# Optimization experiments

Hardware: AMD Instinct MI355X
Metric: run time of the kernel (lower is better)

Reference implementation:

```python
import jax, jax.numpy as jnp
import numpy as np

N_NODES = 100000
N_EDGES = 1600000
N_FEAT = 64
EXP_FEAT = 50
CUTOFF = 5.0
LOG2 = float(np.log(2.0))


def ssp(x):
    # ShiftedSoftplus: softplus(x) - log(2)
    return jax.nn.softplus(x) - LOG2


def setup_inputs() -> dict:
    key = jax.random.key(0)
    ks = jax.random.split(key, 16)
    s = 1.0 / np.sqrt(N_FEAT)
    se = 1.0 / np.sqrt(EXP_FEAT)
    return {
        "neighbour_index": jax.random.randint(ks[0], (2, N_EDGES), 0, N_NODES, dtype=jnp.int64)
        if jax.config.read("jax_enable_x64") else jax.random.randint(ks[0], (2, N_EDGES), 0, N_NODES, dtype=jnp.int32),
        "neighbour_distances": jax.random.uniform(ks[1], (N_EDGES,), jnp.float32) * CUTOFF,
        "node_features": jax.random.normal(ks[2], (N_NODES, N_FEAT), jnp.float32),
        # initial linear transform
        "lin_w": jax.random.uniform(ks[3], (N_FEAT, N_FEAT), jnp.float32, -s, s),
        "lin_b": jax.random.uniform(ks[4], (N_FEAT,), jnp.float32, -s, s),
        # filter MLP: [EXP_FEAT -> N_FEAT -> N_FEAT], ssp between layers
        "f_w1": jax.random.uniform(ks[5], (N_FEAT, EXP_FEAT), jnp.float32, -se, se),
        "f_b1": jax.random.uniform(ks[6], (N_FEAT,), jnp.float32, -se, se),
        "f_w2": jax.random.uniform(ks[7], (N_FEAT, N_FEAT), jnp.float32, -s, s),
        "f_b2": jax.random.uniform(ks[8], (N_FEAT,), jnp.float32, -s, s),
        # output MLP: [N_FEAT -> N_FEAT -> N_FEAT]
        "m_w1": jax.random.uniform(ks[9], (N_FEAT, N_FEAT), jnp.float32, -s, s),
        "m_b1": jax.random.uniform(ks[10], (N_FEAT,), jnp.float32, -s, s),
        "m_w2": jax.random.uniform(ks[11], (N_FEAT, N_FEAT), jnp.float32, -s, s),
        "m_b2": jax.random.uniform(ks[12], (N_FEAT,), jnp.float32, -s, s),
    }


def reference(neighbour_index, neighbour_distances, node_features,
              lin_w, lin_b, f_w1, f_b1, f_w2, f_b2,
              m_w1, m_b1, m_w2, m_b2):
    n_nodes = node_features.shape[0]
    src = neighbour_index[0]  # j (messages gathered from)
    dst = neighbour_index[1]  # i (messages aggregated into)

    # h_i <- W x_i
    h = node_features @ lin_w.T + lin_b  # [N, F]

    # Gaussian smearing of distances: [E, K]
    centers = jnp.linspace(0.0, CUTOFF, EXP_FEAT, dtype=node_features.dtype)
    delta = centers[1] - centers[0]
    coeff = -0.5 / (delta * delta)
    rbf = jnp.exp(coeff * (neighbour_distances[:, None] - centers[None, :]) ** 2)

    # filter MLP F(r_ij): [E, F]
    filt = ssp(rbf @ f_w1.T + f_b1) @ f_w2.T + f_b2

    # message m_ij = h_j * F(r_ij); scatter-add into targets
    msg = h[src] * filt  # [E, F]
    agg = jax.ops.segment_sum(msg, dst, num_segments=n_nodes)  # [N, F]

    # output MLP
    return ssp(agg @ m_w1.T + m_b1) @ m_w2.T + m_b2
```

## Files before the change

### kernel.cpp

```cpp
#include <hip/hip_runtime.h>
#include <hip/hip_fp16.h>

#define NF 64
#define KEXP 50
#define TBL 16384
#define CUTF 5.0f
#define LOG2C 0.6931471805599453f
#define GRP 32
#define GSH 5
#define NSC 256
#define GMAX 4096
#define SCAP 768
#define RPT (SCAP / 256)

typedef unsigned long long ull;
typedef _Float16 f16x8 __attribute__((ext_vector_type(8)));
typedef float f32x4 __attribute__((ext_vector_type(4)));

__device__ __forceinline__ float sspf(float x) {
    return fmaxf(x, 0.0f) + __logf(1.0f + __expf(-fabsf(x))) - LOG2C;
}

__device__ __forceinline__ f16x8 load_wfrag(const float* __restrict__ w, int f, int k0) {
    const float4 q0 = *(const float4*)(w + (size_t)f * NF + k0);
    const float4 q1 = *(const float4*)(w + (size_t)f * NF + k0 + 4);
    f16x8 r;
    r[0] = (_Float16)q0.x; r[1] = (_Float16)q0.y; r[2] = (_Float16)q0.z; r[3] = (_Float16)q0.w;
    r[4] = (_Float16)q1.x; r[5] = (_Float16)q1.y; r[6] = (_Float16)q1.z; r[7] = (_Float16)q1.w;
    return r;
}

__device__ __forceinline__ f16x8 load_afrag_f32(const float* __restrict__ p) {
    const float4 q0 = *(const float4*)(p);
    const float4 q1 = *(const float4*)(p + 4);
    f16x8 r;
    r[0] = (_Float16)q0.x; r[1] = (_Float16)q0.y; r[2] = (_Float16)q0.z; r[3] = (_Float16)q0.w;
    r[4] = (_Float16)q1.x; r[5] = (_Float16)q1.y; r[6] = (_Float16)q1.z; r[7] = (_Float16)q1.w;
    return r;
}

__global__ void __launch_bounds__(256) build_tabnn_k(
    const float* __restrict__ f_w1, const float* __restrict__ f_b1,
    const float* __restrict__ f_w2, const float* __restrict__ f_b2,
    __half* __restrict__ tabnn) {
    const int tid = threadIdx.x;
    const int lane = tid & 63;
    const int wid = tid >> 6;
    float w1r[KEXP], w2r[NF];
    for (int k = 0; k < KEXP; ++k) w1r[k] = f_w1[lane * KEXP + k];
    for (int k = 0; k < NF; ++k)  w2r[k] = f_w2[lane * NF + k];
    const float b1 = f_b1[lane], b2 = f_b2[lane];
    const float delta = CUTF / (float)(KEXP - 1);
    const float coeff = -0.5f / (delta * delta);
    const float dstep = CUTF / (float)(TBL - 1);
    for (int tt = 0; tt < 16; ++tt) {
        const int t = blockIdx.x * 64 + wid * 16 + tt;
        const float d = (float)t * dstep;
        float rbfv = 0.f;
        if (lane < KEXP) {
            const float dd = d - (float)lane * delta;
            rbfv = __expf(coeff * dd * dd);
        }
        float t1 = b1;
        for (int k = 0; k < KEXP; ++k) t1 = fmaf(__shfl(rbfv, k), w1r[k], t1);
        const float sv = sspf(t1);
        float t2 = b2;
        for (int k = 0; k < NF; ++k) t2 = fmaf(__shfl(sv, k), w2r[k], t2);
        tabnn[(size_t)t * NF + lane] = __float2half(t2);
    }
}

__global__ void __launch_bounds__(256) front_k(
    const int* __restrict__ nbr_dst, int n_edges, int ngroups, int chk,
    unsigned* __restrict__ cnt,
    const float* __restrict__ x, const float* __restrict__ w,
    const float* __restrict__ b, __half* __restrict__ h16, int n_nodes)
{
    __shared__ __align__(16) char smem[GMAX * 4];
    const int blk = blockIdx.x;
    const int tid = threadIdx.x;
    const int lane = tid & 63;
    const int wid = tid >> 6;

    if (blk < NSC) {
        unsigned* cnt_s = (unsigned*)smem;
        const int c = blk;
        const int e0 = c * chk;
        const int e1 = min(e0 + chk, n_edges);
        const int m = max(e1 - e0, 0);
        for (int g = tid; g < ngroups; g += 256) cnt_s[g] = 0u;
        __syncthreads();
        for (int i = tid; i < m; i += 256)
            atomicAdd(&cnt_s[(unsigned)nbr_dst[e0 + i] >> GSH], 1u);
        __syncthreads();
        const size_t ob = (size_t)c * ngroups;
        for (int g = tid; g < ngroups; g += 256) cnt[ob + g] = cnt_s[g];
    } else {
        _Float16 (*stile)[16][72] = (_Float16(*)[16][72])smem;
        const int col = lane & 15;
        const int quad = lane >> 4;
        f16x8 bw[4][2];
        float bv[4];
        #pragma unroll
        for (int t = 0; t < 4; ++t) {
            #pragma unroll
            for (int kb = 0; kb < 2; ++kb)
                bw[t][kb] = load_wfrag(w, 16 * t + col, kb * 32 + quad * 8);
            bv[t] = b[16 * t + col];
        }
        const int pb = blk - NSC;
        const int pgrid = gridDim.x - NSC;
        const int ntiles = (n_nodes + 15) >> 4;
        for (int tile = pb * 4 + wid; tile < ntiles; tile += pgrid * 4) {
            const int n0 = tile << 4;
            const int nr = min(n0 + col, n_nodes - 1);
            f16x8 a[2];
            #pragma unroll
            for (int kb = 0; kb < 2; ++kb)
                a[kb] = load_afrag_f32(x + (size_t)nr * NF + kb * 32 + quad * 8);
            f32x4 acc[4];
            #pragma unroll
            for (int t = 0; t < 4; ++t) acc[t] = (f32x4){bv[t], bv[t], bv[t], bv[t]};
            #pragma unroll
            for (int t = 0; t < 4; ++t)
                #pragma unroll
                for (int kb = 0; kb < 2; ++kb)
                    acc[t] = __builtin_amdgcn_mfma_f32_16x16x32_f16(a[kb], bw[t][kb], acc[t], 0, 0, 0);
            #pragma unroll
            for (int t = 0; t < 4; ++t)
                #pragma unroll
                for (int r = 0; r < 4; ++r)
                    stile[wid][quad * 4 + r][16 * t + col] = (_Float16)acc[t][r];
            __threadfence_block();
            #pragma unroll
            for (int it = 0; it < 2; ++it) {
                const int chunk = it * 64 + lane;
                const int row = chunk >> 3;
                const int off = (chunk & 7) * 8;
                const int n = n0 + row;
                if (n < n_nodes)
                    *(uint4*)(h16 + (size_t)n * NF + off) = *(const uint4*)&stile[wid][row][off];
            }
            __threadfence_block();
        }
    }
}

__global__ void __launch_bounds__(64) colscan_k(const unsigned* __restrict__ cnt,
                                                unsigned* __restrict__ colpre,
                                                unsigned* __restrict__ tot, int ngroups) {
    const int g = blockIdx.x;
    const int lane = threadIdx.x;
    unsigned v[4];
    unsigned s = 0u;
    #pragma unroll
    for (int j = 0; j < 4; ++j) {
        v[j] = cnt[(size_t)(4 * lane + j) * ngroups + g];
        s += v[j];
    }
    unsigned run = s;
    #pragma unroll
    for (int d = 1; d < 64; d <<= 1) {
        const unsigned t = __shfl_up(run, d, 64);
        if (lane >= d) run += t;
    }
    unsigned pre = run - s;
    #pragma unroll
    for (int j = 0; j < 4; ++j) {
        colpre[(size_t)(4 * lane + j) * ngroups + g] = pre;
        pre += v[j];
    }
    if (lane == 63) tot[g] = run;
}

__global__ void __launch_bounds__(64) base_k(const unsigned* __restrict__ tot,
                                             unsigned* __restrict__ gbase, int ngroups) {
    const int lane = threadIdx.x;
    unsigned carry = 0u;
    for (int base = 0; base < ngroups; base += 64) {
        const int g = base + lane;
        const unsigned v = (g < ngroups) ? tot[g] : 0u;
        unsigned run = v;
        #pragma unroll
        for (int d = 1; d < 64; d <<= 1) {
            const unsigned t = __shfl_up(run, d, 64);
            if (lane >= d) run += t;
        }
        if (g < ngroups) gbase[g] = carry + run - v;
        carry += (unsigned)__shfl((int)run, 63, 64);
    }
    if (lane == 0) gbase[ngroups] = carry;
}

__global__ void __launch_bounds__(1024) scatter2_k(const int* __restrict__ nbr,
                                                   const float* __restrict__ dist,
                                                   int n_edges, int ngroups, int chk,
                                                   const unsigned* __restrict__ colpre,
                                                   const unsigned* __restrict__ gbase,
                                                   ull* __restrict__ payload) {
    __shared__ unsigned cur_s[GMAX];
    const int tid = threadIdx.x;
    const int c = blockIdx.x;
    const int e0 = c * chk;
    const int e1 = min(e0 + chk, n_edges);
    const int m = max(e1 - e0, 0);
    const size_t ob = (size_t)c * ngroups;
    for (int g = tid; g < ngroups; g += 1024) cur_s[g] = gbase[g] + colpre[ob + g];
    __syncthreads();
    const float scale = (float)(TBL - 1) / CUTF;
    for (int i = tid; i < m; i += 1024) {
        const int e = e0 + i;
        const unsigned dst = (unsigned)nbr[n_edges + e];
        const unsigned src = (unsigned)nbr[e];
        const float xx = dist[e] * scale + 0.5f;
        int i0 = (int)xx;
        i0 = max(0, min(i0, TBL - 1));
        const ull rec = (ull)((unsigned)i0 << 7) |
                        ((ull)((src << 7) | (dst & (GRP - 1u))) << 32);
        const unsigned pos = atomicAdd(&cur_s[dst >> GSH], 1u);
        payload[pos] = rec;
    }
}

__global__ void __launch_bounds__(256) agg_k(
    const ull* __restrict__ payload, const unsigned* __restrict__ gbase,
    const __half* __restrict__ h16, const __half* __restrict__ tabnn,
    float* __restrict__ agg, int n_nodes)
{
    __shared__ ull sorted_s[SCAP];
    __shared__ unsigned cnt_s[GRP];
    __shared__ unsigned base_s[GRP];
    __shared__ unsigned cur_s[GRP];
    const int tid = threadIdx.x;
    const int lane = tid & 63;
    const int wid = tid >> 6;
    const int g = blockIdx.x;
    const unsigned beg = gbase[g];
    const unsigned end = gbase[g + 1];
    const unsigned tot = min(end - beg, (unsigned)SCAP);

    if (tid < GRP) cnt_s[tid] = 0u;
    __syncthreads();
    ull rec[RPT];
    #pragma unroll
    for (int k = 0; k < RPT; ++k) {
        const unsigned i = (unsigned)(k * 256) + tid;
        rec[k] = 0ull;
        if (i < tot) {
            rec[k] = payload[beg + i];
            atomicAdd(&cnt_s[(unsigned)(rec[k] >> 32) & (GRP - 1u)], 1u);
        }
    }
    __syncthreads();
    if (tid < GRP) {
        const unsigned c = cnt_s[tid];
        unsigned run = c;
        #pragma unroll
        for (int d = 1; d < GRP; d <<= 1) {
            const unsigned t = __shfl_up(run, d, 64);
            if (tid >= d) run += t;
        }
        base_s[tid] = run - c;
        cur_s[tid]  = run - c;
    }
    __syncthreads();
    #pragma unroll
    for (int k = 0; k < RPT; ++k) {
        const unsigned i = (unsigned)(k * 256) + tid;
        if (i < tot) {
            const unsigned pos = atomicAdd(&cur_s[(unsigned)(rec[k] >> 32) & (GRP - 1u)], 1u);
            sorted_s[pos] = rec[k];
        }
    }
    __syncthreads();
    const char* tabB = (const char*)tabnn + (lane << 1);
    const char* hB   = (const char*)h16 + (lane << 1);
    auto ev = [&](ull r) -> float {
        const unsigned lo = (unsigned)r;
        const unsigned hi = (unsigned)(r >> 32);
        const float tv = __half2float(*(const __half*)(tabB + lo));
        const float hv = __half2float(*(const __half*)(hB + (hi & 0xFFFFFF80u)));
        return tv * hv;
    };
    const int n0 = g * GRP;
    for (int rr = 0; rr < GRP / 4; ++rr) {
        const int r = wid * (GRP / 4) + rr;
        unsigned i = base_s[r];
        const unsigned e = cur_s[r];
        float acc0 = 0.f, acc1 = 0.f;
        for (; i + 16u <= e; i += 16u) {
            ull rv[16];
            #pragma unroll
            for (int j = 0; j < 16; ++j) rv[j] = sorted_s[i + j];
            float p[16];
            #pragma unroll
            for (int j = 0; j < 16; ++j) p[j] = ev(rv[j]);
            acc0 += ((p[0] + p[1]) + (p[2] + p[3])) + ((p[4] + p[5]) + (p[6] + p[7]));
            acc1 += ((p[8] + p[9]) + (p[10] + p[11])) + ((p[12] + p[13]) + (p[14] + p[15]));
        }
        for (; i + 4u <= e; i += 4u) {
            const ull r0 = sorted_s[i];
            const ull r1 = sorted_s[i + 1];
            const ull r2 = sorted_s[i + 2];
            const ull r3 = sorted_s[i + 3];
            acc0 += ev(r0) + ev(r1);
            acc1 += ev(r2) + ev(r3);
        }
        for (; i < e; ++i) acc0 += ev(sorted_s[i]);
        const int n = n0 + r;
        if (n < n_nodes) agg[(size_t)n * NF + lane] = acc0 + acc1;
    }
}

__global__ void __launch_bounds__(64) oflow2_k(const ull* __restrict__ payload,
                                               const unsigned* __restrict__ gbase,
                                               const __half* __restrict__ h16,
                                               const __half* __restrict__ tabnn,
                                               float* __restrict__ agg) {
    const int g = blockIdx.x;
    const unsigned beg = gbase[g];
    const unsigned end = gbase[g + 1];
    if (end - beg <= (unsigned)SCAP) return;
    const int lane = threadIdx.x;
    const char* tabB = (const char*)tabnn + (lane << 1);
    const char* hB   = (const char*)h16 + (lane << 1);
    for (unsigned i = beg + SCAP; i < end; ++i) {
        const ull rec = payload[i];
        const unsigned lo = (unsigned)rec;
        const unsigned hi = (unsigned)(rec >> 32);
        const float tv = __half2float(*(const __half*)(tabB + lo));
        const float hv = __half2float(*(const __half*)(hB + (hi & 0xFFFFFF80u)));
        const unsigned row = (unsigned)g * GRP + (hi & (GRP - 1u));
        atomicAdd(agg + (size_t)row * NF + lane, tv * hv);
    }
}

__global__ void edge_k(const int* __restrict__ nbr, const float* __restrict__ dist,
                       const __half* __restrict__ h16, const __half* __restrict__ tabnn,
                       float* __restrict__ agg, int n_edges) {
    const int tid = threadIdx.x;
    const int lane = tid & 63;
    const int nwaves = (gridDim.x * blockDim.x) >> 6;
    const int gw = (blockIdx.x * blockDim.x + tid) >> 6;
    const float scale = (float)(TBL - 1) / CUTF;
    const int nbatch = n_edges >> 6;
    for (int bb = gw; bb < nbatch; bb += nwaves) {
        const int e0 = bb << 6;
        int src = nbr[e0 + lane];
        int dst = nbr[n_edges + e0 + lane];
        float d = dist[e0 + lane];
        float xx = d * scale + 0.5f;
        int i0 = (int)xx;
        i0 = max(0, min(i0, TBL - 1));
        #pragma unroll 4
        for (int j = 0; j < 64; ++j) {
            const int sj = __shfl(src, j);
            const int dj = __shfl(dst, j);
            const int ij = __shfl(i0, j);
            const float tv = __half2float(tabnn[(size_t)ij * NF + lane]);
            const float hv = __half2float(h16[(size_t)sj * NF + lane]);
            atomicAdd(agg + (size_t)dj * NF + lane, tv * hv);
        }
    }
    if (gw == 0) {
        for (int e = nbatch << 6; e < n_edges; ++e) {
            const int sj = nbr[e];
            const int dj = nbr[n_edges + e];
            const float d = dist[e];
            float xx = d * scale + 0.5f;
            int ij = (int)xx;
            ij = max(0, min(ij, TBL - 1));
            const float tv = __half2float(tabnn[(size_t)ij * NF + lane]);
            const float hv = __half2float(h16[(size_t)sj * NF + lane]);
            atomicAdd(agg + (size_t)dj * NF + lane, tv * hv);
        }
    }
}

__global__ void __launch_bounds__(256) out_mlp_k(const float* __restrict__ agg,
                                                 const float* __restrict__ w1,
                                                 const float* __restrict__ b1,
                                                 const float* __restrict__ w2,
                                                 const float* __restrict__ b2,
                                                 float* __restrict__ out, int n_nodes) {
    __shared__ _Float16 stile[4][16][72];
    const int tid = threadIdx.x;
    const int lane = tid & 63;
    const int wid = tid >> 6;
    const int col = lane & 15;
    const int quad = lane >> 4;

    f16x8 bw1[4][2], bw2[4][2];
    float b1v[4], b2v[4];
    #pragma unroll
    for (int t = 0; t < 4; ++t) {
        #pragma unroll
        for (int kb = 0; kb < 2; ++kb) {
            bw1[t][kb] = load_wfrag(w1, 16 * t + col, kb * 32 + quad * 8);
            bw2[t][kb] = load_wfrag(w2, 16 * t + col, kb * 32 + quad * 8);
        }
        b1v[t] = b1[16 * t + col];
        b2v[t] = b2[16 * t + col];
    }

    const int ntiles = (n_nodes + 15) >> 4;
    for (int tile = blockIdx.x * 4 + wid; tile < ntiles; tile += gridDim.x * 4) {
        const int n0 = tile << 4;
        const int nr = min(n0 + col, n_nodes - 1);
        f16x8 a[2];
        #pragma unroll
        for (int kb = 0; kb < 2; ++kb)
            a[kb] = load_afrag_f32(agg + (size_t)nr * NF + kb * 32 + quad * 8);
        f32x4 acc[4];
        #pragma unroll
        for (int t = 0; t < 4; ++t) acc[t] = (f32x4){b1v[t], b1v[t], b1v[t], b1v[t]};
        #pragma unroll
        for (int t = 0; t < 4; ++t)
            #pragma unroll
            for (int kb = 0; kb < 2; ++kb)
                acc[t] = __builtin_amdgcn_mfma_f32_16x16x32_f16(a[kb], bw1[t][kb], acc[t], 0, 0, 0);
        #pragma unroll
        for (int t = 0; t < 4; ++t)
            #pragma unroll
            for (int r = 0; r < 4; ++r)
                stile[wid][quad * 4 + r][16 * t + col] = (_Float16)sspf(acc[t][r]);
        __threadfence_block();
        f16x8 a2[2];
        #pragma unroll
        for (int kb = 0; kb < 2; ++kb)
            a2[kb] = *(const f16x8*)&stile[wid][col][kb * 32 + quad * 8];
        f32x4 acc2[4];
        #pragma unroll
        for (int t = 0; t < 4; ++t) acc2[t] = (f32x4){b2v[t], b2v[t], b2v[t], b2v[t]};
        #pragma unroll
        for (int t = 0; t < 4; ++t)
            #pragma unroll
            for (int kb = 0; kb < 2; ++kb)
                acc2[t] = __builtin_amdgcn_mfma_f32_16x16x32_f16(a2[kb], bw2[t][kb], acc2[t], 0, 0, 0);
        #pragma unroll
        for (int t = 0; t < 4; ++t)
            #pragma unroll
            for (int r = 0; r < 4; ++r) {
                const int n = n0 + quad * 4 + r;
                if (n < n_nodes) out[(size_t)n * NF + 16 * t + col] = acc2[t][r];
            }
        __threadfence_block();
    }
}

extern "C" void kernel_launch(void* const* d_in, const int* in_sizes, int n_in,
                              void* d_out, int out_size, void* d_ws, size_t ws_size,
                              hipStream_t stream) {
    const int*   nbr   = (const int*)d_in[0];
    const float* dist  = (const float*)d_in[1];
    const float* x     = (const float*)d_in[2];
    const float* lin_w = (const float*)d_in[3];
    const float* lin_b = (const float*)d_in[4];
    const float* f_w1  = (const float*)d_in[5];
    const float* f_b1  = (const float*)d_in[6];
    const float* f_w2  = (const float*)d_in[7];
    const float* f_b2  = (const float*)d_in[8];
    const float* m_w1  = (const float*)d_in[9];
    const float* m_b1  = (const float*)d_in[10];
    const float* m_w2  = (const float*)d_in[11];
    const float* m_b2  = (const float*)d_in[12];

    const int n_edges = in_sizes[1];
    const int n_nodes = in_sizes[2] / NF;
    const int ngroups = (n_nodes + GRP - 1) / GRP;
    const int chk     = (n_edges + NSC - 1) / NSC;
    const int ntiles  = (n_nodes + 15) / 16;
    const int mlp_blk = (ntiles + 3) / 4;

    float* out = (float*)d_out;
    float* agg = out;

    char* ws = (char*)d_ws;
    size_t off = 0;
    auto alloc = [&](size_t bytes) { char* p = ws + off; off = (off + bytes + 255) & ~(size_t)255; return p; };
    __half*   h16     = (__half*)alloc((size_t)n_nodes * NF * sizeof(__half));
    __half*   tabnn   = (__half*)alloc((size_t)TBL * NF * sizeof(__half));
    unsigned* cnt     = (unsigned*)alloc((size_t)NSC * ngroups * sizeof(unsigned));
    unsigned* colpre  = (unsigned*)alloc((size_t)NSC * ngroups * sizeof(unsigned));
    unsigned* tot     = (unsigned*)alloc((size_t)ngroups * sizeof(unsigned));
    unsigned* gbase   = (unsigned*)alloc((size_t)(ngroups + 1) * sizeof(unsigned));
    ull*      payload = (ull*)alloc((size_t)NSC * chk * sizeof(ull));
    const bool sort_path = (off <= ws_size) && (ngroups <= GMAX) && (n_nodes <= (1 << 17));

    build_tabnn_k<<<TBL / 64, 256, 0, stream>>>(f_w1, f_b1, f_w2, f_b2, tabnn);
    front_k<<<NSC + mlp_blk, 256, 0, stream>>>(
        nbr + n_edges, n_edges, ngroups, chk, cnt,
        x, lin_w, lin_b, h16, n_nodes);

    if (sort_path) {
        colscan_k<<<ngroups, 64, 0, stream>>>(cnt, colpre, tot, ngroups);
        base_k<<<1, 64, 0, stream>>>(tot, gbase, ngroups);
        scatter2_k<<<NSC, 1024, 0, stream>>>(nbr, dist, n_edges, ngroups, chk,
                                             colpre, gbase, payload);
        agg_k<<<ngroups, 256, 0, stream>>>(payload, gbase, h16, tabnn, agg, n_nodes);
        oflow2_k<<<ngroups, 64, 0, stream>>>(payload, gbase, h16, tabnn, agg);
    } else {
        hipMemsetAsync(agg, 0, (size_t)n_nodes * NF * sizeof(float), stream);
        edge_k<<<2048, 256, 0, stream>>>(nbr, dist, h16, tabnn, agg, n_edges);
    }
    out_mlp_k<<<mlp_blk, 256, 0, stream>>>(agg, m_w1, m_b1, m_w2, m_b2, out, n_nodes);
}
```

Before: 193.2 us.

## Fuse output MLP and overflow handling into the aggregation kernel

The aggregation kernel now keeps per-group aggregates in shared memory, folds overflow edges in with shared-memory atomics, and then runs the two-layer output MLP with MFMA on two waves before writing the final output. This removes the separate overflow kernel, the out_mlp kernel launch, and the global write and reread of the aggregate buffer. In exchange, shared memory use per block rises, and only two of four waves do the MLP work, which may lengthen the block tail.

```diff
diff --git a/kernel.cpp b/kernel.cpp
--- a/kernel.cpp
+++ b/kernel.cpp
@@ -30,7 +30,7 @@
     return r;
 }
 
-__device__ __forceinline__ f16x8 load_afrag_f32(const float* __restrict__ p) {
+__device__ __forceinline__ f16x8 load_afrag_f32(const float* p) {
     const float4 q0 = *(const float4*)(p);
     const float4 q1 = *(const float4*)(p + 4);
     f16x8 r;
@@ -222,12 +222,16 @@
     }
 }
 
-__global__ void __launch_bounds__(256) agg_k(
+__global__ void __launch_bounds__(256) agg_mlp_k(
     const ull* __restrict__ payload, const unsigned* __restrict__ gbase,
     const __half* __restrict__ h16, const __half* __restrict__ tabnn,
-    float* __restrict__ agg, int n_nodes)
+    const float* __restrict__ w1, const float* __restrict__ b1,
+    const float* __restrict__ w2, const float* __restrict__ b2,
+    float* __restrict__ out, int n_nodes)
 {
     __shared__ ull sorted_s[SCAP];
+    __shared__ float aggf[GRP][NF + 4];
+    __shared__ _Float16 hs[2][16][72];
     __shared__ unsigned cnt_s[GRP];
     __shared__ unsigned base_s[GRP];
     __shared__ unsigned cur_s[GRP];
@@ -282,7 +286,6 @@
         const float hv = __half2float(*(const __half*)(hB + (hi & 0xFFFFFF80u)));
         return tv * hv;
     };
-    const int n0 = g * GRP;
     for (int rr = 0; rr < GRP / 4; ++rr) {
         const int r = wid * (GRP / 4) + rr;
         unsigned i = base_s[r];
@@ -307,31 +310,70 @@
             acc1 += ev(r2) + ev(r3);
         }
         for (; i < e; ++i) acc0 += ev(sorted_s[i]);
-        const int n = n0 + r;
-        if (n < n_nodes) agg[(size_t)n * NF + lane] = acc0 + acc1;
-    }
-}
-
-__global__ void __launch_bounds__(64) oflow2_k(const ull* __restrict__ payload,
-                                               const unsigned* __restrict__ gbase,
-                                               const __half* __restrict__ h16,
-                                               const __half* __restrict__ tabnn,
-                                               float* __restrict__ agg) {
-    const int g = blockIdx.x;
-    const unsigned beg = gbase[g];
-    const unsigned end = gbase[g + 1];
-    if (end - beg <= (unsigned)SCAP) return;
-    const int lane = threadIdx.x;
-    const char* tabB = (const char*)tabnn + (lane << 1);
-    const char* hB   = (const char*)h16 + (lane << 1);
-    for (unsigned i = beg + SCAP; i < end; ++i) {
-        const ull rec = payload[i];
-        const unsigned lo = (unsigned)rec;
-        const unsigned hi = (unsigned)(rec >> 32);
-        const float tv = __half2float(*(const __half*)(tabB + lo));
-        const float hv = __half2float(*(const __half*)(hB + (hi & 0xFFFFFF80u)));
-        const unsigned row = (unsigned)g * GRP + (hi & (GRP - 1u));
-        atomicAdd(agg + (size_t)row * NF + lane, tv * hv);
+        aggf[r][lane] = acc0 + acc1;
+    }
+    __syncthreads();
+    if (end - beg > (unsigned)SCAP) {
+        for (unsigned i = (unsigned)SCAP + (unsigned)wid; i < end - beg; i += 4u) {
+            const ull r = payload[beg + i];
+            const unsigned row = (unsigned)(r >> 32) & (GRP - 1u);
+            atomicAdd(&aggf[row][lane], ev(r));
+        }
+        __syncthreads();
+    }
+    if (wid < 2) {
+        const int col = lane & 15;
+        const int quad = lane >> 4;
+        f16x8 bw1r[4][2], bw2r[4][2];
+        float b1v[4], b2v[4];
+        #pragma unroll
+        for (int t = 0; t < 4; ++t) {
+            #pragma unroll
+            for (int kb = 0; kb < 2; ++kb) {
+                bw1r[t][kb] = load_wfrag(w1, 16 * t + col, kb * 32 + quad * 8);
+                bw2r[t][kb] = load_wfrag(w2, 16 * t + col, kb * 32 + quad * 8);
+            }
+            b1v[t] = b1[16 * t + col];
+            b2v[t] = b2[16 * t + col];
+        }
+        f16x8 a[2];
+        #pragma unroll
+        for (int kb = 0; kb < 2; ++kb)
+            a[kb] = load_afrag_f32(&aggf[wid * 16 + col][kb * 32 + quad * 8]);
+        f32x4 acc[4];
+        #pragma unroll
+        for (int t = 0; t < 4; ++t) acc[t] = (f32x4){b1v[t], b1v[t], b1v[t], b1v[t]};
+        #pragma unroll
+        for (int t = 0; t < 4; ++t)
+            #pragma unroll
+            for (int kb = 0; kb < 2; ++kb)
+                acc[t] = __builtin_amdgcn_mfma_f32_16x16x32_f16(a[kb], bw1r[t][kb], acc[t], 0, 0, 0);
+        #pragma unroll
+        for (int t = 0; t < 4; ++t)
+            #pragma unroll
+            for (int r = 0; r < 4; ++r)
+                hs[wid][quad * 4 + r][16 * t + col] = (_Float16)sspf(acc[t][r]);
+        __threadfence_block();
+        f16x8 a2[2];
+        #pragma unroll
+        for (int kb = 0; kb < 2; ++kb)
+            a2[kb] = *(const f16x8*)&hs[wid][col][kb * 32 + quad * 8];
+        f32x4 acc2[4];
+        #pragma unroll
+        for (int t = 0; t < 4; ++t) acc2[t] = (f32x4){b2v[t], b2v[t], b2v[t], b2v[t]};
+        #pragma unroll
+        for (int t = 0; t < 4; ++t)
+            #pragma unroll
+            for (int kb = 0; kb < 2; ++kb)
+                acc2[t] = __builtin_amdgcn_mfma_f32_16x16x32_f16(a2[kb], bw2r[t][kb], acc2[t], 0, 0, 0);
+        const int n0 = g * GRP + wid * 16;
+        #pragma unroll
+        for (int t = 0; t < 4; ++t)
+            #pragma unroll
+            for (int r = 0; r < 4; ++r) {
+                const int n = n0 + quad * 4 + r;
+                if (n < n_nodes) out[(size_t)n * NF + 16 * t + col] = acc2[t][r];
+            }
     }
 }
 
@@ -473,7 +515,6 @@
     const int mlp_blk = (ntiles + 3) / 4;
 
     float* out = (float*)d_out;
-    float* agg = out;
 
     char* ws = (char*)d_ws;
     size_t off = 0;
@@ -497,11 +538,12 @@
         base_k<<<1, 64, 0, stream>>>(tot, gbase, ngroups);
         scatter2_k<<<NSC, 1024, 0, stream>>>(nbr, dist, n_edges, ngroups, chk,
                                              colpre, gbase, payload);
-        agg_k<<<ngroups, 256, 0, stream>>>(payload, gbase, h16, tabnn, agg, n_nodes);
-        oflow2_k<<<ngroups, 64, 0, stream>>>(payload, gbase, h16, tabnn, agg);
+        agg_mlp_k<<<ngroups, 256, 0, stream>>>(payload, gbase, h16, tabnn,
+                                               m_w1, m_b1, m_w2, m_b2, out, n_nodes);
     } else {
+        float* agg = out;
         hipMemsetAsync(agg, 0, (size_t)n_nodes * NF * sizeof(float), stream);
         edge_k<<<2048, 256, 0, stream>>>(nbr, dist, h16, tabnn, agg, n_edges);
-    }
-    out_mlp_k<<<mlp_blk, 256, 0, stream>>>(agg, m_w1, m_b1, m_w2, m_b2, out, n_nodes);
-}
+        out_mlp_k<<<mlp_blk, 256, 0, stream>>>(agg, m_w1, m_b1, m_w2, m_b2, out, n_nodes);
+    }
+}
```

New measurement: 215.8 us. +11.7%, slower.
